# Performance work log

Measured on AMD Instinct MI355X. Metric: run time of the kernel, lower is better.

Reference implementation:

```python
import jax, jax.numpy as jnp
import numpy as np
from jax import lax

TOP_K = 6
NORM_MIN = 1e-12


def setup_inputs() -> dict:
    key = jax.random.key(0)
    k0, k1, k2, k3, k4, k5 = jax.random.split(key, 6)
    B, S, H, E, I = 2, 1024, 2048, 64, 512
    return {
        "hidden_states": jax.random.normal(k0, (B, S, H), dtype=jnp.float32),
        "gate_w": jax.random.normal(k1, (E, H), dtype=jnp.float32) * 0.02,
        "e_bias": jax.random.normal(k2, (E,), dtype=jnp.float32) * 0.01,
        "gate_proj": jax.random.normal(k3, (E, H, I), dtype=jnp.float32) * 0.02,
        "up_proj": jax.random.normal(k4, (E, H, I), dtype=jnp.float32) * 0.02,
        "down_proj": jax.random.normal(k5, (E, I, H), dtype=jnp.float32) * 0.02,
    }


def reference(hidden_states, gate_w, e_bias, gate_proj, up_proj, down_proj):
    B, S, H = hidden_states.shape
    E = gate_w.shape[0]
    x = hidden_states.reshape(-1, H)                      # [T, H]
    T = x.shape[0]

    # --- routing (done in float32 in the original) ---
    router_logits = x.astype(jnp.float32) @ gate_w.T      # [T, E]
    routing_probs = jax.nn.softmax(router_logits, axis=-1)
    # topk over bias-corrected scores, but weights come from raw probs
    _, selected = lax.top_k(routing_probs + e_bias[None, :], TOP_K)  # [T, k]
    w = jnp.take_along_axis(routing_probs, selected, axis=-1)        # [T, k]
    w = w / jnp.clip(w.sum(axis=-1, keepdims=True), NORM_MIN)
    w = w.astype(hidden_states.dtype)

    # combine weights: [T, E], zero for unselected experts
    combine = jnp.zeros((T, E), dtype=hidden_states.dtype)
    combine = combine.at[jnp.arange(T)[:, None], selected].add(w)

    # --- experts: SwiGLU MLP per expert, weighted-sum combine ---
    def step(acc, params):
        wg, wu, wd, c = params                            # wg,wu [H,I]; wd [I,H]; c [T]
        h = jax.nn.silu(x @ wg) * (x @ wu)                # [T, I]
        return acc + (h @ wd) * c[:, None], None

    init = jnp.zeros((T, H), dtype=hidden_states.dtype)
    final, _ = lax.scan(step, init, (gate_proj, up_proj, down_proj, combine.T))
    return final.reshape(-1), router_logits.reshape(-1)
```

## Files before the change

### kernel.cpp

```cpp
#include <hip/hip_runtime.h>
#include <math.h>

#define T_TOK 2048
#define H_DIM 2048
#define E_NUM 64
#define I_DIM 512
#define TOPK  6
#define NPAIR (T_TOK * TOPK)
#define MAXTILES 80

typedef __attribute__((ext_vector_type(8))) short s8;
typedef __attribute__((ext_vector_type(4))) float f4;
typedef __attribute__((ext_vector_type(8))) unsigned short u16x8;

static __device__ __forceinline__ unsigned short f2bf(float f) {
  unsigned int u = __float_as_uint(f);
  u += 0x7fff + ((u >> 16) & 1);
  return (unsigned short)(u >> 16);
}
static __device__ __forceinline__ unsigned int cvt_pk(float lo, float hi) {
  unsigned int r;
  asm("v_cvt_pk_bf16_f32 %0, %1, %2" : "=v"(r) : "v"(lo), "v"(hi));
  return r;
}
static __device__ __forceinline__ void gload_lds16(const void* g, void* l) {
  __builtin_amdgcn_global_load_lds(
      (const __attribute__((address_space(1))) unsigned int*)g,
      (__attribute__((address_space(3))) unsigned int*)l, 16, 0, 0);
}
#define SBAR()      __builtin_amdgcn_s_barrier()
#define SCHED0()    __builtin_amdgcn_sched_barrier(0)
#define PRIO1()     __builtin_amdgcn_s_setprio(1)
#define PRIO0()     __builtin_amdgcn_s_setprio(0)
#define WAIT_LGKM0() asm volatile("s_waitcnt lgkmcnt(0)" ::: "memory")
#define WAIT_VM0()   asm volatile("s_waitcnt vmcnt(0)" ::: "memory")
#define WAIT_VM4()   asm volatile("s_waitcnt vmcnt(4)" ::: "memory")
#define WAIT_VM6()   asm volatile("s_waitcnt vmcnt(6)" ::: "memory")

__global__ __launch_bounds__(512) void router_kernel(
    const float* __restrict__ x, const float* __restrict__ gw,
    const float* __restrict__ ebias, float* __restrict__ logits_out,
    int* __restrict__ sel, float* __restrict__ wsel)
{
  __shared__ float xs[4][H_DIM];
  __shared__ float lg[4][E_NUM];
  int t0 = blockIdx.x * 4;
  int tid = threadIdx.x;
  {
    float4* xsv = (float4*)&xs[0][0];
    const float4* src = (const float4*)(x + (size_t)t0 * H_DIM);
    for (int i = tid; i < 4 * H_DIM / 4; i += 512) xsv[i] = src[i];
  }
  __syncthreads();

  int wave = tid >> 6, lane = tid & 63;
  for (int ii = 0; ii < 4; ++ii) {
    int e0 = wave * 8 + ii * 2, e1 = e0 + 1;
    const float4* g0 = (const float4*)(gw + (size_t)e0 * H_DIM);
    const float4* g1 = (const float4*)(gw + (size_t)e1 * H_DIM);
    float s00=0.f,s01=0.f,s02=0.f,s03=0.f, s10=0.f,s11=0.f,s12=0.f,s13=0.f;
    for (int h4 = lane; h4 < H_DIM / 4; h4 += 64) {
      float4 w0 = g0[h4], w1 = g1[h4];
      float4 a0 = ((const float4*)xs[0])[h4];
      float4 a1 = ((const float4*)xs[1])[h4];
      float4 a2 = ((const float4*)xs[2])[h4];
      float4 a3 = ((const float4*)xs[3])[h4];
      s00 += w0.x*a0.x + w0.y*a0.y + w0.z*a0.z + w0.w*a0.w;
      s01 += w0.x*a1.x + w0.y*a1.y + w0.z*a1.z + w0.w*a1.w;
      s02 += w0.x*a2.x + w0.y*a2.y + w0.z*a2.z + w0.w*a2.w;
      s03 += w0.x*a3.x + w0.y*a3.y + w0.z*a3.z + w0.w*a3.w;
      s10 += w1.x*a0.x + w1.y*a0.y + w1.z*a0.z + w1.w*a0.w;
      s11 += w1.x*a1.x + w1.y*a1.y + w1.z*a1.z + w1.w*a1.w;
      s12 += w1.x*a2.x + w1.y*a2.y + w1.z*a2.z + w1.w*a2.w;
      s13 += w1.x*a3.x + w1.y*a3.y + w1.z*a3.z + w1.w*a3.w;
    }
    for (int off = 32; off; off >>= 1) {
      s00 += __shfl_down(s00, off); s01 += __shfl_down(s01, off);
      s02 += __shfl_down(s02, off); s03 += __shfl_down(s03, off);
      s10 += __shfl_down(s10, off); s11 += __shfl_down(s11, off);
      s12 += __shfl_down(s12, off); s13 += __shfl_down(s13, off);
    }
    if (lane == 0) {
      lg[0][e0]=s00; lg[1][e0]=s01; lg[2][e0]=s02; lg[3][e0]=s03;
      lg[0][e1]=s10; lg[1][e1]=s11; lg[2][e1]=s12; lg[3][e1]=s13;
    }
  }
  __syncthreads();

  if (tid < 256) {
    int tt = tid >> 6, e = tid & 63;
    logits_out[(size_t)(t0 + tt) * E_NUM + e] = lg[tt][e];
  }

  if (wave == 0) {
    for (int tt = 0; tt < 4; ++tt) {
      int t = t0 + tt;
      float v = lg[tt][lane];
      float m = v;
      for (int off = 32; off; off >>= 1) m = fmaxf(m, __shfl_xor(m, off));
      float ex = __expf(v - m);
      float sum = ex;
      for (int off = 32; off; off >>= 1) sum += __shfl_xor(sum, off);
      float prob = ex / sum;
      float sc = prob + ebias[lane];

      int selidx[TOPK]; float selw[TOPK]; float wsum = 0.f;
      #pragma unroll
      for (int k = 0; k < TOPK; ++k) {
        float mm = sc;
        for (int off = 32; off; off >>= 1) mm = fmaxf(mm, __shfl_xor(mm, off));
        unsigned long long ball = __ballot(sc == mm);
        int s = __ffsll(ball) - 1;
        float p = __shfl(prob, s);
        selidx[k] = s; selw[k] = p; wsum += p;
        if (lane == s) sc = -INFINITY;
      }
      if (lane == 0) {
        float inv = 1.f / fmaxf(wsum, 1e-12f);
        #pragma unroll
        for (int k = 0; k < TOPK; ++k) {
          sel[t * TOPK + k] = selidx[k];
          wsel[t * TOPK + k] = selw[k] * inv;
        }
      }
    }
  }
}

__global__ __launch_bounds__(64) void build_lists(
    const int* __restrict__ sel, const float* __restrict__ wsel,
    int* __restrict__ cnt, int* __restrict__ toklist, float* __restrict__ wtlist)
{
  int e = blockIdx.x, lane = threadIdx.x;
  int base = 0;
  for (int t0 = 0; t0 < T_TOK; t0 += 64) {
    int t = t0 + lane;
    int flag = 0; float w = 0.f;
    #pragma unroll
    for (int k = 0; k < TOPK; ++k)
      if (sel[t * TOPK + k] == e) { flag = 1; w = wsel[t * TOPK + k]; }
    unsigned long long b = __ballot(flag);
    int pos = base + __popcll(b & ((1ull << lane) - 1ull));
    if (flag) { toklist[e * T_TOK + pos] = t; wtlist[e * T_TOK + pos] = w; }
    base += __popcll(b);
  }
  if (lane == 0) cnt[e] = base;
}

__global__ void scan_kernel(const int* __restrict__ cnt,
                            int* __restrict__ tmap, int* __restrict__ ntile) {
  if (threadIdx.x == 0) {
    int nt = 0;
    for (int e = 0; e < E_NUM; ++e) {
      int m = (cnt[e] + 255) >> 8;
      for (int tb = 0; tb < m && nt < MAXTILES; ++tb) tmap[nt++] = e * 16 + tb;
    }
    *ntile = nt;
  }
}

__global__ __launch_bounds__(256) void permute_kernel(
    const float* __restrict__ x, const int* __restrict__ cnt,
    const int* __restrict__ toklist, const int* __restrict__ tmap,
    const int* __restrict__ ntile, unsigned short* __restrict__ xt)
{
  int tile = blockIdx.y;
  if (tile >= *ntile) return;
  int ks = blockIdx.x;
  int em = tmap[tile], e = em >> 4, tb = em & 15;
  int n = cnt[e];
  int r = threadIdx.x;
  int tok = toklist[e * T_TOK + min(tb * 256 + r, n - 1)];
  const float4* src = (const float4*)(x + (size_t)tok * H_DIM + ks * 32);
  float4 v[8];
  #pragma unroll
  for (int q = 0; q < 8; ++q) v[q] = src[q];
  int g = (r >> 1) & 3;
  unsigned short* dst = xt + ((size_t)(tile * 64 + ks) * 1024 + r * 4) * 8;
  #pragma unroll
  for (int u = 0; u < 4; ++u) {
    int k16 = u ^ g;
    float4 a = v[2 * k16], b = v[2 * k16 + 1];
    u16x8 p;
    ((unsigned int*)&p)[0] = cvt_pk(a.x, a.y);
    ((unsigned int*)&p)[1] = cvt_pk(a.z, a.w);
    ((unsigned int*)&p)[2] = cvt_pk(b.x, b.y);
    ((unsigned int*)&p)[3] = cvt_pk(b.z, b.w);
    *(u16x8*)(dst + u * 8) = p;
  }
}

__global__ __launch_bounds__(512, 4) void gateup_kernel(
    const unsigned short* __restrict__ xt, const float* __restrict__ gp,
    const float* __restrict__ up, const int* __restrict__ tmap,
    const int* __restrict__ ntile, unsigned short* __restrict__ hat)
{
  __shared__ __align__(16) unsigned short A_lds[3][8192];
  __shared__ __align__(16) unsigned int   Bt[2][2][64 * 20];
  int tile = blockIdx.x;
  if (tile >= *ntile) return;
  int e = tmap[tile] >> 4;
  int ic = blockIdx.y, colbase = ic * 64;
  int tid = threadIdx.x, lane = tid & 63, wave = tid >> 6;
  int matc = wave >> 2, cw = wave & 3;
  int lrow = (lane >> 4) * 4, lcol = lane & 15, kgl = lane >> 4;
  int hp = tid & 15, cb = (tid >> 4) & 15, mstage = tid >> 8;
  const float* bsrc0 = ((mstage == 0) ? gp : up)
      + (size_t)e * (H_DIM * I_DIM) + colbase + (size_t)(2 * hp) * I_DIM + cb * 4;
  const unsigned short* achunk0 = xt + (size_t)tile * 64 * 1024 * 8;

  f4 acc[4][4];
  #pragma unroll
  for (int a = 0; a < 4; ++a)
    #pragma unroll
    for (int b = 0; b < 4; ++b) acc[a][b] = (f4)0.f;

  float4 p0, p1, q0, q1;
  {
    const unsigned short* s = achunk0 + (size_t)(wave * 128 + lane) * 8;
    gload_lds16(s,       &A_lds[0][(wave * 128) * 8]);
    gload_lds16(s + 512, &A_lds[0][(wave * 128 + 64) * 8]);
    p0 = *(const float4*)bsrc0;
    p1 = *(const float4*)(bsrc0 + I_DIM);
    WAIT_VM0();
    unsigned int* db = &Bt[0][mstage][cb * 4 * 20 + hp];
    db[0]  = cvt_pk(p0.x, p1.x); db[20] = cvt_pk(p0.y, p1.y);
    db[40] = cvt_pk(p0.z, p1.z); db[60] = cvt_pk(p0.w, p1.w);
    const unsigned short* s1 = achunk0 + (size_t)(1024 + wave * 128 + lane) * 8;
    gload_lds16(s1,       &A_lds[1][(wave * 128) * 8]);
    gload_lds16(s1 + 512, &A_lds[1][(wave * 128 + 64) * 8]);
    const float* b1 = bsrc0 + (size_t)32 * I_DIM;
    p0 = *(const float4*)b1;
    p1 = *(const float4*)(b1 + I_DIM);
    WAIT_LGKM0();
    SBAR();
    SCHED0();
  }

#define GU_STEP(K, C0, C1, N0, N1) do {                                            \
    if ((K) + 2 < 64) {                                                            \
      int ab = ((K) + 2) % 3;                                                      \
      const unsigned short* s = achunk0 + ((size_t)((K) + 2) * 1024 + wave * 128 + lane) * 8; \
      gload_lds16(s,       &A_lds[ab][(wave * 128) * 8]);                          \
      gload_lds16(s + 512, &A_lds[ab][(wave * 128 + 64) * 8]);                     \
      const float* b = bsrc0 + (size_t)((K) + 2) * 32 * I_DIM;                     \
      N0 = *(const float4*)b; N1 = *(const float4*)(b + I_DIM);                    \
      WAIT_VM4();                                                                  \
    } else { WAIT_VM0(); }                                                         \
    if ((K) + 1 < 64) {                                                            \
      unsigned int* db = &Bt[((K) + 1) & 1][mstage][cb * 4 * 20 + hp];             \
      db[0]  = cvt_pk(C0.x, C1.x); db[20] = cvt_pk(C0.y, C1.y);                    \
      db[40] = cvt_pk(C0.z, C1.z); db[60] = cvt_pk(C0.w, C1.w);                    \
    }                                                                              \
    {                                                                              \
      int ab = (K) % 3;                                                            \
      s8 afr[4];                                                                   \
      _Pragma("unroll")                                                            \
      for (int mf = 0; mf < 4; ++mf) {                                             \
        int r = cw * 64 + mf * 16 + lcol;                                          \
        afr[mf] = *(s8*)&A_lds[ab][r * 32 + ((kgl ^ ((r >> 1) & 3)) * 8)];         \
      }                                                                            \
      PRIO1();                                                                     \
      _Pragma("unroll")                                                            \
      for (int nf = 0; nf < 4; ++nf) {                                             \
        s8 bfr = *(s8*)&Bt[(K) & 1][matc][(nf * 16 + lcol) * 20 + kgl * 4];        \
        _Pragma("unroll")                                                          \
        for (int mf = 0; mf < 4; ++mf)                                             \
          acc[mf][nf] = __builtin_amdgcn_mfma_f32_16x16x32_bf16(afr[mf], bfr, acc[mf][nf], 0, 0, 0); \
      }                                                                            \
      PRIO0();                                                                     \
    }                                                                              \
    if ((K) + 1 < 64) { WAIT_LGKM0(); SBAR(); SCHED0(); }                          \
  } while (0)

  for (int k = 0; k < 64; k += 2) {
    GU_STEP(k,     p0, p1, q0, q1);
    GU_STEP(k + 1, q0, q1, p0, p1);
  }
#undef GU_STEP

  f4* exch = (f4*)&Bt[0][0][0];
  unsigned short* hs = &A_lds[0][0];
  #pragma unroll
  for (int nf = 0; nf < 4; ++nf) {
    __syncthreads();
    if (wave >= 4) {
      #pragma unroll
      for (int mf = 0; mf < 4; ++mf)
        exch[((wave - 4) * 4 + mf) * 64 + lane] = acc[mf][nf];
    }
    __syncthreads();
    if (wave < 4) {
      #pragma unroll
      for (int mf = 0; mf < 4; ++mf) {
        f4 u = exch[(wave * 4 + mf) * 64 + lane];
        #pragma unroll
        for (int j = 0; j < 4; ++j) {
          float g = acc[mf][nf][j];
          float h = g / (1.f + __expf(-g)) * u[j];
          hs[(wave * 64 + mf * 16 + lrow + j) * 64 + nf * 16 + lcol] = f2bf(h);
        }
      }
    }
  }
  __syncthreads();
  #pragma unroll
  for (int c = 0; c < 2; ++c) {
    unsigned short* base = hat + (size_t)(tile * 16 + ic * 2 + c) * 1024 * 8;
    for (int uu = tid; uu < 1024; uu += 512) {
      int row = uu >> 2, k16 = (uu & 3) ^ ((row >> 1) & 3);
      *(u16x8*)(base + (size_t)uu * 8) = *(const u16x8*)&hs[row * 64 + c * 32 + k16 * 8];
    }
  }
}

__global__ __launch_bounds__(256, 4) void down_kernel(
    const unsigned short* __restrict__ hat, const float* __restrict__ dp,
    const int* __restrict__ cnt, const int* __restrict__ tmap,
    const int* __restrict__ ntile, const int* __restrict__ toklist,
    const float* __restrict__ wtlist, float* __restrict__ out)
{
  __shared__ __align__(16) unsigned short A_lds[3][8192];
  __shared__ __align__(16) unsigned int   Bt[2][64 * 20];
  __shared__ int   stok[256];
  __shared__ float swt[256];
  int tile = blockIdx.x;
  if (tile >= *ntile) return;
  int em = tmap[tile], e = em >> 4, tb = em & 15;
  int n = cnt[e];
  int hc = blockIdx.y, colbase = hc * 64;
  int tid = threadIdx.x, lane = tid & 63, wave = tid >> 6, wbase = wave * 64;
  int lrow = (lane >> 4) * 4, lcol = lane & 15, kgl = lane >> 4;
  int hp = tid & 15, cb = tid >> 4;
  const float* bsrc0 = dp + (size_t)e * (I_DIM * H_DIM) + colbase
                       + (size_t)(2 * hp) * H_DIM + cb * 4;
  const unsigned short* achunk0 = hat + (size_t)tile * 16 * 1024 * 8;

  int rr = tb * 256 + tid;
  stok[tid] = (rr < n) ? toklist[e * T_TOK + rr] : 0;
  swt[tid]  = (rr < n) ? wtlist[e * T_TOK + rr] : 0.f;

  f4 acc[4][4];
  #pragma unroll
  for (int a = 0; a < 4; ++a)
    #pragma unroll
    for (int b = 0; b < 4; ++b) acc[a][b] = (f4)0.f;

  float4 p0, p1, q0, q1;
  {
    const unsigned short* s = achunk0 + (size_t)(wave * 256 + lane) * 8;
    #pragma unroll
    for (int i = 0; i < 4; ++i)
      gload_lds16(s + i * 512, &A_lds[0][(wave * 256 + i * 64) * 8]);
    p0 = *(const float4*)bsrc0;
    p1 = *(const float4*)(bsrc0 + H_DIM);
    WAIT_VM0();
    unsigned int* db = &Bt[0][cb * 4 * 20 + hp];
    db[0]  = cvt_pk(p0.x, p1.x); db[20] = cvt_pk(p0.y, p1.y);
    db[40] = cvt_pk(p0.z, p1.z); db[60] = cvt_pk(p0.w, p1.w);
    const unsigned short* s1 = achunk0 + (size_t)(1024 + wave * 256 + lane) * 8;
    #pragma unroll
    for (int i = 0; i < 4; ++i)
      gload_lds16(s1 + i * 512, &A_lds[1][(wave * 256 + i * 64) * 8]);
    const float* b1 = bsrc0 + (size_t)32 * H_DIM;
    p0 = *(const float4*)b1;
    p1 = *(const float4*)(b1 + H_DIM);
    WAIT_LGKM0();
    SBAR();
    SCHED0();
  }

#define DN_STEP(K, C0, C1, N0, N1) do {                                            \
    if ((K) + 2 < 16) {                                                            \
      int ab = ((K) + 2) % 3;                                                      \
      const unsigned short* s = achunk0 + ((size_t)((K) + 2) * 1024 + wave * 256 + lane) * 8; \
      _Pragma("unroll")                                                            \
      for (int i = 0; i < 4; ++i)                                                  \
        gload_lds16(s + i * 512, &A_lds[ab][(wave * 256 + i * 64) * 8]);           \
      const float* b = bsrc0 + (size_t)((K) + 2) * 32 * H_DIM;                     \
      N0 = *(const float4*)b; N1 = *(const float4*)(b + H_DIM);                    \
      WAIT_VM6();                                                                  \
    } else { WAIT_VM0(); }                                                         \
    if ((K) + 1 < 16) {                                                            \
      unsigned int* db = &Bt[((K) + 1) & 1][cb * 4 * 20 + hp];                     \
      db[0]  = cvt_pk(C0.x, C1.x); db[20] = cvt_pk(C0.y, C1.y);                    \
      db[40] = cvt_pk(C0.z, C1.z); db[60] = cvt_pk(C0.w, C1.w);                    \
    }                                                                              \
    {                                                                              \
      int ab = (K) % 3;                                                            \
      s8 afr[4];                                                                   \
      _Pragma("unroll")                                                            \
      for (int mf = 0; mf < 4; ++mf) {                                             \
        int r = wbase + mf * 16 + lcol;                                            \
        afr[mf] = *(s8*)&A_lds[ab][r * 32 + ((kgl ^ ((r >> 1) & 3)) * 8)];         \
      }                                                                            \
      PRIO1();                                                                     \
      _Pragma("unroll")                                                            \
      for (int nf = 0; nf < 4; ++nf) {                                             \
        s8 bfr = *(s8*)&Bt[(K) & 1][(nf * 16 + lcol) * 20 + kgl * 4];              \
        _Pragma("unroll")                                                          \
        for (int mf = 0; mf < 4; ++mf)                                             \
          acc[mf][nf] = __builtin_amdgcn_mfma_f32_16x16x32_bf16(afr[mf], bfr, acc[mf][nf], 0, 0, 0); \
      }                                                                            \
      PRIO0();                                                                     \
    }                                                                              \
    if ((K) + 1 < 16) { WAIT_LGKM0(); SBAR(); SCHED0(); }                          \
  } while (0)

  for (int k = 0; k < 16; k += 2) {
    DN_STEP(k,     p0, p1, q0, q1);
    DN_STEP(k + 1, q0, q1, p0, p1);
  }
#undef DN_STEP

  #pragma unroll
  for (int mf = 0; mf < 4; ++mf)
    #pragma unroll
    for (int nf = 0; nf < 4; ++nf)
      #pragma unroll
      for (int j = 0; j < 4; ++j) {
        int r = wbase + mf * 16 + lrow + j;
        if (tb * 256 + r < n)
          atomicAdd(&out[(size_t)stok[r] * H_DIM + colbase + nf * 16 + lcol],
                    acc[mf][nf][j] * swt[r]);
      }
}

extern "C" void kernel_launch(void* const* d_in, const int* in_sizes, int n_in,
                              void* d_out, int out_size, void* d_ws, size_t ws_size,
                              hipStream_t stream) {
  const float* hidden = (const float*)d_in[0];
  const float* gate_w = (const float*)d_in[1];
  const float* e_bias = (const float*)d_in[2];
  const float* gate_p = (const float*)d_in[3];
  const float* up_p   = (const float*)d_in[4];
  const float* down_p = (const float*)d_in[5];

  float* out_final  = (float*)d_out;
  float* out_logits = out_final + (size_t)T_TOK * H_DIM;

  int*   cnt     = (int*)d_ws;
  int*   texp    = cnt + 64;
  int*   ntile   = texp + 64;
  int*   tmap    = ntile + 16;
  int*   sel     = tmap + MAXTILES;
  float* wsel    = (float*)(sel + NPAIR);
  int*   toklist = (int*)(wsel + NPAIR);
  float* wtlist  = (float*)(toklist + E_NUM * T_TOK);
  unsigned short* xt  = (unsigned short*)(wtlist + E_NUM * T_TOK);
  unsigned short* hat = xt + (size_t)MAXTILES * 64 * 1024 * 8;

  hipMemsetAsync(out_final, 0, (size_t)T_TOK * H_DIM * sizeof(float), stream);

  router_kernel<<<T_TOK / 4, 512, 0, stream>>>(hidden, gate_w, e_bias, out_logits, sel, wsel);
  build_lists<<<E_NUM, 64, 0, stream>>>(sel, wsel, cnt, toklist, wtlist);
  scan_kernel<<<1, 64, 0, stream>>>(cnt, tmap, ntile);
  permute_kernel<<<dim3(64, MAXTILES), 256, 0, stream>>>(hidden, cnt, toklist, tmap, ntile, xt);
  gateup_kernel<<<dim3(MAXTILES, I_DIM / 64), 512, 0, stream>>>(
      xt, gate_p, up_p, tmap, ntile, hat);
  down_kernel<<<dim3(MAXTILES, H_DIM / 64), 256, 0, stream>>>(
      hat, down_p, cnt, tmap, ntile, toklist, wtlist, out_final);
}
```

Before: 563.5 us.

## Switch A-tile LDS pipeline from triple to double buffering and drop setprio

In both the gate/up and down expert GEMM kernels, the A-operand LDS staging goes from three buffers with a two-step lookahead to two buffers with a one-step lookahead. The vmcnt waits are reworked so the next A tile is loaded during the current step's MFMAs and waited on before the barrier. The s_setprio hints around the MFMA blocks are also removed. This cuts LDS use per block, which may allow more resident blocks, but it shortens the prefetch distance for the A tiles and risks exposing global-to-LDS load latency.

```diff
diff --git a/kernel.cpp b/kernel.cpp
--- a/kernel.cpp
+++ b/kernel.cpp
@@ -30,10 +30,9 @@
 }
 #define SBAR()      __builtin_amdgcn_s_barrier()
 #define SCHED0()    __builtin_amdgcn_sched_barrier(0)
-#define PRIO1()     __builtin_amdgcn_s_setprio(1)
-#define PRIO0()     __builtin_amdgcn_s_setprio(0)
 #define WAIT_LGKM0() asm volatile("s_waitcnt lgkmcnt(0)" ::: "memory")
 #define WAIT_VM0()   asm volatile("s_waitcnt vmcnt(0)" ::: "memory")
+#define WAIT_VM2()   asm volatile("s_waitcnt vmcnt(2)" ::: "memory")
 #define WAIT_VM4()   asm volatile("s_waitcnt vmcnt(4)" ::: "memory")
 #define WAIT_VM6()   asm volatile("s_waitcnt vmcnt(6)" ::: "memory")
 
@@ -195,7 +194,7 @@
     const float* __restrict__ up, const int* __restrict__ tmap,
     const int* __restrict__ ntile, unsigned short* __restrict__ hat)
 {
-  __shared__ __align__(16) unsigned short A_lds[3][8192];
+  __shared__ __align__(16) unsigned short A_lds[2][8192];
   __shared__ __align__(16) unsigned int   Bt[2][2][64 * 20];
   int tile = blockIdx.x;
   if (tile >= *ntile) return;
@@ -226,41 +225,39 @@
     unsigned int* db = &Bt[0][mstage][cb * 4 * 20 + hp];
     db[0]  = cvt_pk(p0.x, p1.x); db[20] = cvt_pk(p0.y, p1.y);
     db[40] = cvt_pk(p0.z, p1.z); db[60] = cvt_pk(p0.w, p1.w);
-    const unsigned short* s1 = achunk0 + (size_t)(1024 + wave * 128 + lane) * 8;
-    gload_lds16(s1,       &A_lds[1][(wave * 128) * 8]);
-    gload_lds16(s1 + 512, &A_lds[1][(wave * 128 + 64) * 8]);
     const float* b1 = bsrc0 + (size_t)32 * I_DIM;
-    p0 = *(const float4*)b1;
-    p1 = *(const float4*)(b1 + I_DIM);
+    q0 = *(const float4*)b1;
+    q1 = *(const float4*)(b1 + I_DIM);
     WAIT_LGKM0();
     SBAR();
     SCHED0();
   }
 
 #define GU_STEP(K, C0, C1, N0, N1) do {                                            \
+    if ((K) + 1 < 64) {                                                            \
+      const unsigned short* s = achunk0 + ((size_t)((K) + 1) * 1024 + wave * 128 + lane) * 8; \
+      gload_lds16(s,       &A_lds[((K) + 1) & 1][(wave * 128) * 8]);               \
+      gload_lds16(s + 512, &A_lds[((K) + 1) & 1][(wave * 128 + 64) * 8]);          \
+    }                                                                              \
     if ((K) + 2 < 64) {                                                            \
-      int ab = ((K) + 2) % 3;                                                      \
-      const unsigned short* s = achunk0 + ((size_t)((K) + 2) * 1024 + wave * 128 + lane) * 8; \
-      gload_lds16(s,       &A_lds[ab][(wave * 128) * 8]);                          \
-      gload_lds16(s + 512, &A_lds[ab][(wave * 128 + 64) * 8]);                     \
       const float* b = bsrc0 + (size_t)((K) + 2) * 32 * I_DIM;                     \
       N0 = *(const float4*)b; N1 = *(const float4*)(b + I_DIM);                    \
-      WAIT_VM4();                                                                  \
-    } else { WAIT_VM0(); }                                                         \
+    }                                                                              \
+    if ((K) + 2 < 64)      { WAIT_VM4(); }                                         \
+    else if ((K) + 1 < 64) { WAIT_VM2(); }                                         \
+    else                   { WAIT_VM0(); }                                         \
     if ((K) + 1 < 64) {                                                            \
       unsigned int* db = &Bt[((K) + 1) & 1][mstage][cb * 4 * 20 + hp];             \
       db[0]  = cvt_pk(C0.x, C1.x); db[20] = cvt_pk(C0.y, C1.y);                    \
       db[40] = cvt_pk(C0.z, C1.z); db[60] = cvt_pk(C0.w, C1.w);                    \
     }                                                                              \
     {                                                                              \
-      int ab = (K) % 3;                                                            \
       s8 afr[4];                                                                   \
       _Pragma("unroll")                                                            \
       for (int mf = 0; mf < 4; ++mf) {                                             \
         int r = cw * 64 + mf * 16 + lcol;                                          \
-        afr[mf] = *(s8*)&A_lds[ab][r * 32 + ((kgl ^ ((r >> 1) & 3)) * 8)];         \
+        afr[mf] = *(s8*)&A_lds[(K) & 1][r * 32 + ((kgl ^ ((r >> 1) & 3)) * 8)];    \
       }                                                                            \
-      PRIO1();                                                                     \
       _Pragma("unroll")                                                            \
       for (int nf = 0; nf < 4; ++nf) {                                             \
         s8 bfr = *(s8*)&Bt[(K) & 1][matc][(nf * 16 + lcol) * 20 + kgl * 4];        \
@@ -268,14 +265,16 @@
         for (int mf = 0; mf < 4; ++mf)                                             \
           acc[mf][nf] = __builtin_amdgcn_mfma_f32_16x16x32_bf16(afr[mf], bfr, acc[mf][nf], 0, 0, 0); \
       }                                                                            \
-      PRIO0();                                                                     \
-    }                                                                              \
-    if ((K) + 1 < 64) { WAIT_LGKM0(); SBAR(); SCHED0(); }                          \
+    }                                                                              \
+    if ((K) + 1 < 64) {                                                            \
+      if ((K) + 2 < 64) { WAIT_VM2(); } else { WAIT_VM0(); }                       \
+      WAIT_LGKM0(); SBAR(); SCHED0();                                              \
+    }                                                                              \
   } while (0)
 
   for (int k = 0; k < 64; k += 2) {
-    GU_STEP(k,     p0, p1, q0, q1);
-    GU_STEP(k + 1, q0, q1, p0, p1);
+    GU_STEP(k,     q0, q1, p0, p1);
+    GU_STEP(k + 1, p0, p1, q0, q1);
   }
 #undef GU_STEP
 
@@ -320,7 +319,7 @@
     const int* __restrict__ ntile, const int* __restrict__ toklist,
     const float* __restrict__ wtlist, float* __restrict__ out)
 {
-  __shared__ __align__(16) unsigned short A_lds[3][8192];
+  __shared__ __align__(16) unsigned short A_lds[2][8192];
   __shared__ __align__(16) unsigned int   Bt[2][64 * 20];
   __shared__ int   stok[256];
   __shared__ float swt[256];
@@ -358,43 +357,40 @@
     unsigned int* db = &Bt[0][cb * 4 * 20 + hp];
     db[0]  = cvt_pk(p0.x, p1.x); db[20] = cvt_pk(p0.y, p1.y);
     db[40] = cvt_pk(p0.z, p1.z); db[60] = cvt_pk(p0.w, p1.w);
-    const unsigned short* s1 = achunk0 + (size_t)(1024 + wave * 256 + lane) * 8;
-    #pragma unroll
-    for (int i = 0; i < 4; ++i)
-      gload_lds16(s1 + i * 512, &A_lds[1][(wave * 256 + i * 64) * 8]);
     const float* b1 = bsrc0 + (size_t)32 * H_DIM;
-    p0 = *(const float4*)b1;
-    p1 = *(const float4*)(b1 + H_DIM);
+    q0 = *(const float4*)b1;
+    q1 = *(const float4*)(b1 + H_DIM);
     WAIT_LGKM0();
     SBAR();
     SCHED0();
   }
 
 #define DN_STEP(K, C0, C1, N0, N1) do {                                            \
-    if ((K) + 2 < 16) {                                                            \
-      int ab = ((K) + 2) % 3;                                                      \
-      const unsigned short* s = achunk0 + ((size_t)((K) + 2) * 1024 + wave * 256 + lane) * 8; \
+    if ((K) + 1 < 16) {                                                            \
+      const unsigned short* s = achunk0 + ((size_t)((K) + 1) * 1024 + wave * 256 + lane) * 8; \
       _Pragma("unroll")                                                            \
       for (int i = 0; i < 4; ++i)                                                  \
-        gload_lds16(s + i * 512, &A_lds[ab][(wave * 256 + i * 64) * 8]);           \
+        gload_lds16(s + i * 512, &A_lds[((K) + 1) & 1][(wave * 256 + i * 64) * 8]);\
+    }                                                                              \
+    if ((K) + 2 < 16) {                                                            \
       const float* b = bsrc0 + (size_t)((K) + 2) * 32 * H_DIM;                     \
       N0 = *(const float4*)b; N1 = *(const float4*)(b + H_DIM);                    \
-      WAIT_VM6();                                                                  \
-    } else { WAIT_VM0(); }                                                         \
+    }                                                                              \
+    if ((K) + 2 < 16)      { WAIT_VM6(); }                                         \
+    else if ((K) + 1 < 16) { WAIT_VM4(); }                                         \
+    else                   { WAIT_VM0(); }                                         \
     if ((K) + 1 < 16) {                                                            \
       unsigned int* db = &Bt[((K) + 1) & 1][cb * 4 * 20 + hp];                     \
       db[0]  = cvt_pk(C0.x, C1.x); db[20] = cvt_pk(C0.y, C1.y);                    \
       db[40] = cvt_pk(C0.z, C1.z); db[60] = cvt_pk(C0.w, C1.w);                    \
     }                                                                              \
     {                                                                              \
-      int ab = (K) % 3;                                                            \
       s8 afr[4];                                                                   \
       _Pragma("unroll")                                                            \
       for (int mf = 0; mf < 4; ++mf) {                                             \
         int r = wbase + mf * 16 + lcol;                                            \
-        afr[mf] = *(s8*)&A_lds[ab][r * 32 + ((kgl ^ ((r >> 1) & 3)) * 8)];         \
+        afr[mf] = *(s8*)&A_lds[(K) & 1][r * 32 + ((kgl ^ ((r >> 1) & 3)) * 8)];    \
       }                                                                            \
-      PRIO1();                                                                     \
       _Pragma("unroll")                                                            \
       for (int nf = 0; nf < 4; ++nf) {                                             \
         s8 bfr = *(s8*)&Bt[(K) & 1][(nf * 16 + lcol) * 20 + kgl * 4];              \
@@ -402,14 +398,16 @@
         for (int mf = 0; mf < 4; ++mf)                                             \
           acc[mf][nf] = __builtin_amdgcn_mfma_f32_16x16x32_bf16(afr[mf], bfr, acc[mf][nf], 0, 0, 0); \
       }                                                                            \
-      PRIO0();                                                                     \
-    }                                                                              \
-    if ((K) + 1 < 16) { WAIT_LGKM0(); SBAR(); SCHED0(); }                          \
+    }                                                                              \
+    if ((K) + 1 < 16) {                                                            \
+      if ((K) + 2 < 16) { WAIT_VM2(); } else { WAIT_VM0(); }                       \
+      WAIT_LGKM0(); SBAR(); SCHED0();                                              \
+    }                                                                              \
   } while (0)
 
   for (int k = 0; k < 16; k += 2) {
-    DN_STEP(k,     p0, p1, q0, q1);
-    DN_STEP(k + 1, q0, q1, p0, p1);
+    DN_STEP(k,     q0, q1, p0, p1);
+    DN_STEP(k + 1, p0, p1, q0, q1);
   }
 #undef DN_STEP
 
```

After: 569.4 us. About the same (+1.1%).
